# Performance work log

Hardware: AMD Instinct MI355X
Metric: run time of the kernel (lower is better)

Reference implementation:

```python
import jax, jax.numpy as jnp
import numpy as np

IN_DIM, H, E_DIM = 32, 64, 16
N_NODES, N_EDGES = 50000, 100000


def setup_inputs() -> dict:
    key = jax.random.key(0)
    ks = jax.random.split(key, 12)
    x = jax.random.normal(ks[0], (N_NODES, IN_DIM), dtype=jnp.float32)
    edge_index = jax.random.randint(ks[1], (2, N_EDGES), 0, N_NODES, dtype=jnp.int64)
    edge_attr = jax.random.uniform(ks[2], (N_EDGES, E_DIM), dtype=jnp.float32)
    def lin(k, fan_in, shape):
        return jax.random.normal(k, shape, dtype=jnp.float32) / np.sqrt(fan_in)
    return {
        "x": x,
        "edge_index": edge_index,
        "edge_attr": edge_attr,
        # lin0: Linear(in_dim, h)
        "lin0_w": lin(ks[3], IN_DIM, (H, IN_DIM)),
        "lin0_b": jnp.zeros((H,), jnp.float32),
        # NNConv's edge network: Linear(edge_dim, h*h)
        "nn_w": lin(ks[4], E_DIM, (H * H, E_DIM)),
        "nn_b": jnp.zeros((H * H,), jnp.float32),
        # NNConv root weight [in_ch, out_ch] and bias
        "root": lin(ks[5], H, (H, H)),
        "conv_b": jnp.zeros((H,), jnp.float32),
        # GRU (single layer): weight_ih [3h,h], weight_hh [3h,h], biases [3h]
        "w_ih": lin(ks[6], H, (3 * H, H)),
        "w_hh": lin(ks[7], H, (3 * H, H)),
        "b_ih": jnp.zeros((3 * H,), jnp.float32),
        "b_hh": jnp.zeros((3 * H,), jnp.float32),
    }


def _nnconv(x, src, dst, edge_attr, nn_w, nn_b, root, conv_b, num_nodes):
    # per-edge weight matrices [E, h_in, h_out] from the edge MLP
    W_e = (edge_attr @ nn_w.T + nn_b).reshape(-1, H, H)
    # gather source features, per-edge matvec, scatter-add to destinations
    msg = jnp.einsum('ei,eio->eo', x[src], W_e)          # [E, h]
    agg = jax.ops.segment_sum(msg, dst, num_segments=num_nodes)
    return agg + x @ root + conv_b


def _gru_step(x, h, w_ih, w_hh, b_ih, b_hh):
    gi = x @ w_ih.T + b_ih                                # [N, 3h]
    gh = h @ w_hh.T + b_hh
    i_r, i_z, i_n = jnp.split(gi, 3, axis=-1)
    h_r, h_z, h_n = jnp.split(gh, 3, axis=-1)
    r = jax.nn.sigmoid(i_r + h_r)
    z = jax.nn.sigmoid(i_z + h_z)
    n = jnp.tanh(i_n + r * h_n)
    return (1.0 - z) * n + z * h


def reference(x, edge_index, edge_attr, lin0_w, lin0_b, nn_w, nn_b,
              root, conv_b, w_ih, w_hh, b_ih, b_hh):
    src, dst = edge_index[0], edge_index[1]
    num_nodes = x.shape[0]
    out = jax.nn.relu(x @ lin0_w.T + lin0_b)              # [N, h]
    h = out
    for _ in range(3):
        m = jax.nn.relu(_nnconv(out, src, dst, edge_attr, nn_w, nn_b,
                                root, conv_b, num_nodes))
        h = _gru_step(m, h, w_ih, w_hh, b_ih, b_hh)
        out = h
    return out
```

## Files before the change

kernel.cpp:

```cpp
#include <hip/hip_runtime.h>
#include <hip/hip_bf16.h>

typedef unsigned short u16;
typedef __attribute__((ext_vector_type(8))) _Float16 h8v;
typedef __attribute__((ext_vector_type(4))) float f32x4;

#define CAP 32

static __device__ __forceinline__ u16 f2h(float f) {
    _Float16 h = (_Float16)f;
    u16 r; __builtin_memcpy(&r, &h, 2); return r;
}
static __device__ __forceinline__ float h2f(u16 b) {
    _Float16 h; __builtin_memcpy(&h, &b, 2); return (float)h;
}
static __device__ __forceinline__ float sigm(float x) {
    return 1.f / (1.f + __expf(-x));
}
static __device__ __forceinline__ float tanh_f(float x) {
    return 1.f - 2.f / (__expf(2.f * x) + 1.f);
}

__global__ __launch_bounds__(256) void k_prep(
        const float* __restrict__ nn_w, const float* __restrict__ nn_b,
        const float* __restrict__ root, const float* __restrict__ w_hh,
        const float* __restrict__ w_ih, const float* __restrict__ lin0_w,
        const float* __restrict__ ea,
        u16* __restrict__ wf2, u16* __restrict__ w1, u16* __restrict__ w2,
        u16* __restrict__ w0, u16* __restrict__ ea16, int* __restrict__ deg,
        int N, int nEA) {
    int idx = blockIdx.x * 256 + threadIdx.x;
    if (idx < 34 * 4 * 512) {
        int j = idx & 7, lane = (idx >> 3) & 63;
        int rest = idx >> 9;
        int ct = rest & 3, kc = rest >> 2;
        int kappa = kc * 32 + ((lane >> 4) * 8) + j;
        int o = ct * 16 + (lane & 15);
        float v;
        if (kappa < 1024) {
            int k = kappa >> 6, i = kappa & 63;
            v = nn_w[(size_t)(i * 64 + o) * 16 + k];
        } else {
            v = nn_b[(size_t)(kappa - 1024) * 64 + o];
        }
        wf2[idx] = f2h(v);
    }
    if (idx < 16384 + 12288 + 2048) {
        if (idx < 16384) {
            int j = idx & 7, lane = (idx >> 3) & 63;
            int rest = idx >> 9;
            int ct = rest & 15, kc = rest >> 4;
            int k = kc * 32 + ((lane >> 4) * 8) + j;
            int col = ct * 16 + (lane & 15);
            float v = (col < 64) ? root[(size_t)k * 64 + col]
                                 : w_hh[(size_t)(col - 64) * 64 + k];
            w1[idx] = f2h(v);
        } else if (idx < 16384 + 12288) {
            int i2 = idx - 16384;
            int j = i2 & 7, lane = (i2 >> 3) & 63;
            int rest = i2 >> 9;
            int ct = rest % 12, kc = rest / 12;
            int k = kc * 32 + ((lane >> 4) * 8) + j;
            int col = ct * 16 + (lane & 15);
            w2[i2] = f2h(w_ih[(size_t)col * 64 + k]);
        } else {
            int i3 = idx - 16384 - 12288;
            int j = i3 & 7, lane = (i3 >> 3) & 63;
            int ct = i3 >> 9;
            int k = ((lane >> 4) * 8) + j;
            int col = ct * 16 + (lane & 15);
            w0[i3] = f2h(lin0_w[(size_t)col * 32 + k]);
        }
    }
    if (idx < N) deg[idx] = 0;
    if (idx < nEA) ea16[idx] = f2h(ea[idx]);
}

__global__ __launch_bounds__(256) void k_build(
        const int* __restrict__ ei, int* __restrict__ deg,
        int* __restrict__ tab, int E) {
    int e = blockIdx.x * 256 + threadIdx.x;
    if (e < E) {
        int dst = ei[E + e];
        int pos = atomicAdd(&deg[dst], 1);
        if (pos < CAP) tab[(size_t)dst * CAP + pos] = e;
    }
}

__global__ __launch_bounds__(256) void k_lin0(
        const float* __restrict__ x, const u16* __restrict__ w0,
        const float* __restrict__ b, float* __restrict__ out, int N) {
    int t = threadIdx.x, l = t & 63, w = t >> 6, g = l >> 4;
    int n0 = blockIdx.x * 64 + w * 16;
    int node = n0 + (l & 15);
    int nc = node < N ? node : N - 1;
    const float* xrow = x + (size_t)nc * 32 + g * 8;
    float4 xa = *(const float4*)(xrow);
    float4 xb = *(const float4*)(xrow + 4);
    h8v xh;
    xh[0] = (_Float16)xa.x; xh[1] = (_Float16)xa.y;
    xh[2] = (_Float16)xa.z; xh[3] = (_Float16)xa.w;
    xh[4] = (_Float16)xb.x; xh[5] = (_Float16)xb.y;
    xh[6] = (_Float16)xb.z; xh[7] = (_Float16)xb.w;

    f32x4 acc[4];
    #pragma unroll
    for (int ct = 0; ct < 4; ct++) {
        h8v wh = *(const h8v*)((const _Float16*)w0 + (ct * 64 + l) * 8);
        acc[ct] = __builtin_amdgcn_mfma_f32_16x16x32_f16(wh, xh, (f32x4)(0.f), 0, 0, 0);
    }
    if (node < N) {
        #pragma unroll
        for (int ct = 0; ct < 4; ct++) {
            int c = ct * 16 + g * 4;
            f32x4 bb = *(const f32x4*)(b + c);
            f32x4 ov;
            #pragma unroll
            for (int r = 0; r < 4; r++) ov[r] = fmaxf(acc[ct][r] + bb[r], 0.f);
            *(f32x4*)(out + (size_t)node * 64 + c) = ov;
        }
    }
}

__global__ __launch_bounds__(256) void k_AB(
        const float* __restrict__ x, const u16* __restrict__ ea16,
        const u16* __restrict__ wf2, const int* __restrict__ ei,
        u16* __restrict__ msg, int E) {
    int t = threadIdx.x, l = t & 63, w = t >> 6, g = l >> 4;
    int eblk = blockIdx.x * 256 + w * 64;

    int eact[4];
    h8v xf0[4], xf1[4], eav[4][2];
    #pragma unroll
    for (int et = 0; et < 4; et++) {
        int e = eblk + et * 16 + (l & 15);
        eact[et] = e;
        int ec = e < E ? e : E - 1;
        int src = ei[ec];
        const float* xr = x + (size_t)src * 64 + g * 8;
        float4 v0 = *(const float4*)(xr);
        float4 v1 = *(const float4*)(xr + 4);
        float4 v2 = *(const float4*)(xr + 32);
        float4 v3 = *(const float4*)(xr + 36);
        h8v a, b;
        a[0] = (_Float16)v0.x; a[1] = (_Float16)v0.y;
        a[2] = (_Float16)v0.z; a[3] = (_Float16)v0.w;
        a[4] = (_Float16)v1.x; a[5] = (_Float16)v1.y;
        a[6] = (_Float16)v1.z; a[7] = (_Float16)v1.w;
        b[0] = (_Float16)v2.x; b[1] = (_Float16)v2.y;
        b[2] = (_Float16)v2.z; b[3] = (_Float16)v2.w;
        b[4] = (_Float16)v3.x; b[5] = (_Float16)v3.y;
        b[6] = (_Float16)v3.z; b[7] = (_Float16)v3.w;
        xf0[et] = a;
        xf1[et] = b;
        const _Float16* ep = (const _Float16*)ea16 + (size_t)ec * 16;
        eav[et][0] = *(const h8v*)(ep);
        eav[et][1] = *(const h8v*)(ep + 8);
    }

    f32x4 acc[4][4];
    #pragma unroll
    for (int et = 0; et < 4; et++)
        #pragma unroll
        for (int ct = 0; ct < 4; ct++) acc[et][ct] = (f32x4)(0.f);

    const _Float16* wfh = (const _Float16*)wf2;

    #pragma unroll
    for (int p = 0; p < 8; p++) {
        #pragma unroll
        for (int kcl = 0; kcl < 4; kcl++) {
            int kc = p * 4 + kcl;
            h8v af[4];
            #pragma unroll
            for (int ct = 0; ct < 4; ct++)
                af[ct] = *(const h8v*)(wfh + (size_t)(kc * 4 + ct) * 512 + l * 8);
            #pragma unroll
            for (int et = 0; et < 4; et++) {
                _Float16 s = (kcl < 2) ? eav[et][p >> 2][(2 * p) & 7]
                                       : eav[et][p >> 2][(2 * p + 1) & 7];
                h8v es = {s, s, s, s, s, s, s, s};
                h8v zf = es * ((kcl & 1) ? xf1[et] : xf0[et]);
                #pragma unroll
                for (int ct = 0; ct < 4; ct++)
                    acc[et][ct] = __builtin_amdgcn_mfma_f32_16x16x32_f16(af[ct], zf, acc[et][ct], 0, 0, 0);
            }
        }
    }
    #pragma unroll
    for (int kcl = 0; kcl < 2; kcl++) {
        int kc = 32 + kcl;
        h8v af[4];
        #pragma unroll
        for (int ct = 0; ct < 4; ct++)
            af[ct] = *(const h8v*)(wfh + (size_t)(kc * 4 + ct) * 512 + l * 8);
        #pragma unroll
        for (int et = 0; et < 4; et++) {
            h8v zf = (kcl & 1) ? xf1[et] : xf0[et];
            #pragma unroll
            for (int ct = 0; ct < 4; ct++)
                acc[et][ct] = __builtin_amdgcn_mfma_f32_16x16x32_f16(af[ct], zf, acc[et][ct], 0, 0, 0);
        }
    }

    #pragma unroll
    for (int et = 0; et < 4; et++) {
        int e = eact[et];
        if (e < E) {
            u16* mr = msg + (size_t)e * 64 + g * 4;
            #pragma unroll
            for (int ct = 0; ct < 4; ct++) {
                ushort4 pk;
                pk.x = f2h(acc[et][ct][0]);
                pk.y = f2h(acc[et][ct][1]);
                pk.z = f2h(acc[et][ct][2]);
                pk.w = f2h(acc[et][ct][3]);
                *(ushort4*)(mr + ct * 16) = pk;
            }
        }
    }
}

__global__ __launch_bounds__(256) void k_C(
        const float* __restrict__ x, const u16* __restrict__ msg,
        const int* __restrict__ deg, const int* __restrict__ tab,
        const u16* __restrict__ w1, const u16* __restrict__ w2,
        const float* __restrict__ conv_b, const float* __restrict__ b_hh,
        const float* __restrict__ b_ih, float* __restrict__ hout, int N) {
    __shared__ float mld[4][16][68];
    int t = threadIdx.x, l = t & 63, w = t >> 6, g = l >> 4;
    int n0 = blockIdx.x * 64 + w * 16;
    int node = n0 + (l & 15);
    int nc = node < N ? node : N - 1;
    const float* xrow = x + (size_t)nc * 64 + g * 8;
    const _Float16* w1h = (const _Float16*)w1;
    const _Float16* w2h = (const _Float16*)w2;

    h8v xh[2];
    #pragma unroll
    for (int kc = 0; kc < 2; kc++) {
        f32x4 a = *(const f32x4*)(xrow + kc * 32);
        f32x4 b = *(const f32x4*)(xrow + kc * 32 + 4);
        #pragma unroll
        for (int j = 0; j < 8; j++) xh[kc][j] = (_Float16)(j < 4 ? a[j] : b[j - 4]);
    }

    f32x4 avs[4];
    #pragma unroll
    for (int ct = 0; ct < 4; ct++) avs[ct] = (f32x4)(0.f);
    if (node < N) {
        int dg = deg[node];
        dg = dg < CAP ? dg : CAP;
        const int* tr = tab + (size_t)node * CAP;
        for (int j = 0; j < dg; j++) {
            int eid = tr[j];
            const u16* mr = msg + (size_t)eid * 64 + g * 4;
            #pragma unroll
            for (int ct = 0; ct < 4; ct++) {
                ushort4 mv = *(const ushort4*)(mr + ct * 16);
                avs[ct][0] += h2f(mv.x);
                avs[ct][1] += h2f(mv.y);
                avs[ct][2] += h2f(mv.z);
                avs[ct][3] += h2f(mv.w);
            }
        }
    }

    f32x4 acc1[16];
    #pragma unroll
    for (int ct = 0; ct < 16; ct++) acc1[ct] = (f32x4)(0.f);
    #pragma unroll
    for (int kc = 0; kc < 2; kc++) {
        #pragma unroll
        for (int ct = 0; ct < 16; ct++) {
            h8v wh = *(const h8v*)(w1h + (size_t)(kc * 16 + ct) * 512 + l * 8);
            acc1[ct] = __builtin_amdgcn_mfma_f32_16x16x32_f16(wh, xh[kc], acc1[ct], 0, 0, 0);
        }
    }

    #pragma unroll
    for (int ct = 0; ct < 4; ct++) {
        int c = ct * 16 + g * 4;
        f32x4 cb = *(const f32x4*)(conv_b + c);
        f32x4 mv;
        #pragma unroll
        for (int r = 0; r < 4; r++) mv[r] = fmaxf(acc1[ct][r] + avs[ct][r] + cb[r], 0.f);
        *(f32x4*)(&mld[w][l & 15][c]) = mv;
    }
    #pragma unroll
    for (int ct = 4; ct < 16; ct++) {
        int c = (ct - 4) * 16 + g * 4;
        f32x4 bh = *(const f32x4*)(b_hh + c);
        #pragma unroll
        for (int r = 0; r < 4; r++) acc1[ct][r] += bh[r];
    }
    __syncthreads();

    h8v mh[2];
    #pragma unroll
    for (int kc = 0; kc < 2; kc++) {
        const float* mr = &mld[w][l & 15][kc * 32 + g * 8];
        f32x4 a = *(const f32x4*)(mr);
        f32x4 b = *(const f32x4*)(mr + 4);
        #pragma unroll
        for (int j = 0; j < 8; j++) mh[kc][j] = (_Float16)(j < 4 ? a[j] : b[j - 4]);
    }

    f32x4 acc2[12];
    #pragma unroll
    for (int ct = 0; ct < 12; ct++) acc2[ct] = (f32x4)(0.f);
    #pragma unroll
    for (int kc = 0; kc < 2; kc++) {
        #pragma unroll
        for (int ct = 0; ct < 12; ct++) {
            h8v wh = *(const h8v*)(w2h + (size_t)(kc * 12 + ct) * 512 + l * 8);
            acc2[ct] = __builtin_amdgcn_mfma_f32_16x16x32_f16(wh, mh[kc], acc2[ct], 0, 0, 0);
        }
    }

    #pragma unroll
    for (int q = 0; q < 4; q++) {
        int c = q * 16 + g * 4;
        f32x4 bir = *(const f32x4*)(b_ih + c);
        f32x4 biz = *(const f32x4*)(b_ih + 64 + c);
        f32x4 bin = *(const f32x4*)(b_ih + 128 + c);
        f32x4 hv = (f32x4)(0.f);
        if (node < N) hv = *(const f32x4*)(x + (size_t)node * 64 + c);
        f32x4 outv;
        #pragma unroll
        for (int r = 0; r < 4; r++) {
            float rr = sigm(acc2[q][r] + bir[r] + acc1[4 + q][r]);
            float zz = sigm(acc2[4 + q][r] + biz[r] + acc1[8 + q][r]);
            float nt = tanh_f(acc2[8 + q][r] + bin[r] + rr * acc1[12 + q][r]);
            outv[r] = (1.f - zz) * nt + zz * hv[r];
        }
        if (node < N) *(f32x4*)(hout + (size_t)node * 64 + c) = outv;
    }
}

extern "C" void kernel_launch(void* const* d_in, const int* in_sizes, int n_in,
                              void* d_out, int out_size, void* d_ws, size_t ws_size,
                              hipStream_t stream) {
    const float* x_in   = (const float*)d_in[0];
    const int*   ei     = (const int*)d_in[1];
    const float* ea     = (const float*)d_in[2];
    const float* lin0_w = (const float*)d_in[3];
    const float* lin0_b = (const float*)d_in[4];
    const float* nn_w   = (const float*)d_in[5];
    const float* nn_b   = (const float*)d_in[6];
    const float* root   = (const float*)d_in[7];
    const float* conv_b = (const float*)d_in[8];
    const float* w_ih   = (const float*)d_in[9];
    const float* w_hh   = (const float*)d_in[10];
    const float* b_ih   = (const float*)d_in[11];
    const float* b_hh   = (const float*)d_in[12];

    int N = in_sizes[0] / 32;
    int E = in_sizes[1] / 2;

    char* ws = (char*)d_ws;
    size_t off = 0;
    auto alloc = [&](size_t bytes) { char* p = ws + off; off += (bytes + 255) & ~(size_t)255; return p; };
    float* xbuf   = (float*)alloc((size_t)N * 64 * 4);
    u16*   msg    = (u16*)alloc((size_t)E * 64 * 2);
    u16*   wf2    = (u16*)alloc((size_t)34 * 4 * 512 * 2);
    u16*   ea16   = (u16*)alloc((size_t)E * 16 * 2);
    u16*   w1     = (u16*)alloc(16384 * 2);
    u16*   w2     = (u16*)alloc(12288 * 2);
    u16*   w0     = (u16*)alloc(2048 * 2);
    int*   deg    = (int*)alloc((size_t)N * 4);
    int*   tab    = (int*)alloc((size_t)N * CAP * 4);
    (void)ws_size;

    int nEA = E * 16;
    hipLaunchKernelGGL(k_prep, dim3((nEA + 255) / 256), dim3(256), 0, stream,
                       nn_w, nn_b, root, w_hh, w_ih, lin0_w, ea,
                       wf2, w1, w2, w0, ea16, deg, N, nEA);
    hipLaunchKernelGGL(k_build, dim3((E + 255) / 256), dim3(256), 0, stream, ei, deg, tab, E);
    hipLaunchKernelGGL(k_lin0, dim3((N + 63) / 64), dim3(256), 0, stream, x_in, w0, lin0_b, xbuf, N);

    for (int it = 0; it < 3; it++) {
        hipLaunchKernelGGL(k_AB, dim3((E + 255) / 256), dim3(256), 0, stream,
                           xbuf, ea16, wf2, ei, msg, E);
        float* hout = (it == 2) ? (float*)d_out : xbuf;
        hipLaunchKernelGGL(k_C, dim3((N + 63) / 64), dim3(256), 0, stream, xbuf, msg,
                           deg, tab, w1, w2, conv_b, b_hh, b_ih, hout, N);
    }
}
```

Measured before the change: 178.0 us.

## Stage edge-network weights through LDS with register prefetch in k_AB

The edge-message kernel now copies the fused edge-network weight tiles from global memory into a 16KB shared-memory buffer in chunks. The next chunk is prefetched into registers while MFMAs consume the current one, and each wave reads its A fragments from LDS instead of global/L2. Each wave now handles 32 edges instead of 64, halving accumulators and doubling the grid. The goal is to reduce redundant global weight loads and register pressure, at the cost of two block barriers per chunk and less weight reuse per wave.

```diff
diff --git a/kernel.cpp b/kernel.cpp
--- a/kernel.cpp
+++ b/kernel.cpp
@@ -126,13 +126,14 @@
         const float* __restrict__ x, const u16* __restrict__ ea16,
         const u16* __restrict__ wf2, const int* __restrict__ ei,
         u16* __restrict__ msg, int E) {
+    __shared__ __align__(16) u16 Ab[8192];
     int t = threadIdx.x, l = t & 63, w = t >> 6, g = l >> 4;
-    int eblk = blockIdx.x * 256 + w * 64;
-
-    int eact[4];
-    h8v xf0[4], xf1[4], eav[4][2];
-    #pragma unroll
-    for (int et = 0; et < 4; et++) {
+    int eblk = blockIdx.x * 128 + w * 32;
+
+    int eact[2];
+    h8v xf0[2], xf1[2], eav[2][2];
+    #pragma unroll
+    for (int et = 0; et < 2; et++) {
         int e = eblk + et * 16 + (l & 15);
         eact[et] = e;
         int ec = e < E ? e : E - 1;
@@ -158,27 +159,45 @@
         eav[et][1] = *(const h8v*)(ep + 8);
     }
 
-    f32x4 acc[4][4];
-    #pragma unroll
-    for (int et = 0; et < 4; et++)
+    f32x4 acc[2][4];
+    #pragma unroll
+    for (int et = 0; et < 2; et++)
         #pragma unroll
         for (int ct = 0; ct < 4; ct++) acc[et][ct] = (f32x4)(0.f);
 
-    const _Float16* wfh = (const _Float16*)wf2;
+    const uint4* wf2u = (const uint4*)wf2;
+    uint4* Abu = (uint4*)Ab;
+    const _Float16* AbH = (const _Float16*)Ab;
+
+    {
+        uint4 s0[4];
+        #pragma unroll
+        for (int i = 0; i < 4; i++) s0[i] = wf2u[t + i * 256];
+        #pragma unroll
+        for (int i = 0; i < 4; i++) Abu[t + i * 256] = s0[i];
+    }
+    __syncthreads();
 
     #pragma unroll
     for (int p = 0; p < 8; p++) {
+        uint4 st[4];
+        if (p < 7) {
+            #pragma unroll
+            for (int i = 0; i < 4; i++) st[i] = wf2u[(p + 1) * 1024 + t + i * 256];
+        } else {
+            st[0] = wf2u[8 * 1024 + t];
+            st[1] = wf2u[8 * 1024 + 256 + t];
+        }
         #pragma unroll
         for (int kcl = 0; kcl < 4; kcl++) {
-            int kc = p * 4 + kcl;
             h8v af[4];
             #pragma unroll
             for (int ct = 0; ct < 4; ct++)
-                af[ct] = *(const h8v*)(wfh + (size_t)(kc * 4 + ct) * 512 + l * 8);
-            #pragma unroll
-            for (int et = 0; et < 4; et++) {
-                _Float16 s = (kcl < 2) ? eav[et][p >> 2][(2 * p) & 7]
-                                       : eav[et][p >> 2][(2 * p + 1) & 7];
+                af[ct] = *(const h8v*)(AbH + (kcl * 4 + ct) * 512 + l * 8);
+            const int k = 2 * p + (kcl >> 1);
+            #pragma unroll
+            for (int et = 0; et < 2; et++) {
+                _Float16 s = eav[et][k >> 3][k & 7];
                 h8v es = {s, s, s, s, s, s, s, s};
                 h8v zf = es * ((kcl & 1) ? xf1[et] : xf0[et]);
                 #pragma unroll
@@ -186,16 +205,25 @@
                     acc[et][ct] = __builtin_amdgcn_mfma_f32_16x16x32_f16(af[ct], zf, acc[et][ct], 0, 0, 0);
             }
         }
-    }
+        __syncthreads();
+        if (p < 7) {
+            #pragma unroll
+            for (int i = 0; i < 4; i++) Abu[t + i * 256] = st[i];
+        } else {
+            Abu[t] = st[0];
+            Abu[256 + t] = st[1];
+        }
+        __syncthreads();
+    }
+
     #pragma unroll
     for (int kcl = 0; kcl < 2; kcl++) {
-        int kc = 32 + kcl;
         h8v af[4];
         #pragma unroll
         for (int ct = 0; ct < 4; ct++)
-            af[ct] = *(const h8v*)(wfh + (size_t)(kc * 4 + ct) * 512 + l * 8);
-        #pragma unroll
-        for (int et = 0; et < 4; et++) {
+            af[ct] = *(const h8v*)(AbH + (kcl * 4 + ct) * 512 + l * 8);
+        #pragma unroll
+        for (int et = 0; et < 2; et++) {
             h8v zf = (kcl & 1) ? xf1[et] : xf0[et];
             #pragma unroll
             for (int ct = 0; ct < 4; ct++)
@@ -204,7 +232,7 @@
     }
 
     #pragma unroll
-    for (int et = 0; et < 4; et++) {
+    for (int et = 0; et < 2; et++) {
         int e = eact[et];
         if (e < E) {
             u16* mr = msg + (size_t)e * 64 + g * 4;
@@ -380,7 +408,7 @@
     hipLaunchKernelGGL(k_lin0, dim3((N + 63) / 64), dim3(256), 0, stream, x_in, w0, lin0_b, xbuf, N);
 
     for (int it = 0; it < 3; it++) {
-        hipLaunchKernelGGL(k_AB, dim3((E + 255) / 256), dim3(256), 0, stream,
+        hipLaunchKernelGGL(k_AB, dim3((E + 127) / 128), dim3(256), 0, stream,
                            xbuf, ea16, wf2, ei, msg, E);
         float* hout = (it == 2) ? (float*)d_out : xbuf;
         hipLaunchKernelGGL(k_C, dim3((N + 63) / 64), dim3(256), 0, stream, xbuf, msg,
```

New measurement: 240.5 us. 1.35x slower.

## Fuse per-edge message compute into node aggregation+GRU kernel via shared-memory tiles

Applied to the files above, without the earlier changes.

Fuses the edge-message kernel and the node aggregation/GRU kernel into one per-node-tile kernel. Each block prefix-sums the degrees of its 64 nodes and computes the messages for their incoming edges with MFMA into an LDS tile, then reduces them without going through a global msg buffer. It also merges the edge-table build and lin0 kernels into one launch, and ping-pongs node buffers so reads and writes do not alias. This removes the global message round-trip and some launches. In exchange it adds block syncs, a serial edge-list fill done by one wavefront, per-block load imbalance, and fewer blocks (N/64) doing the edge MFMA work.

```diff
diff --git a/kernel.cpp b/kernel.cpp
--- a/kernel.cpp
+++ b/kernel.cpp
@@ -6,6 +6,7 @@
 typedef __attribute__((ext_vector_type(4))) float f32x4;
 
 #define CAP 32
+#define ECAP 256
 
 static __device__ __forceinline__ u16 f2h(float f) {
     _Float16 h = (_Float16)f;
@@ -76,25 +77,29 @@
     if (idx < nEA) ea16[idx] = f2h(ea[idx]);
 }
 
-__global__ __launch_bounds__(256) void k_build(
-        const int* __restrict__ ei, int* __restrict__ deg,
-        int* __restrict__ tab, int E) {
-    int e = blockIdx.x * 256 + threadIdx.x;
-    if (e < E) {
-        int dst = ei[E + e];
-        int pos = atomicAdd(&deg[dst], 1);
-        if (pos < CAP) tab[(size_t)dst * CAP + pos] = e;
-    }
-}
-
-__global__ __launch_bounds__(256) void k_lin0(
-        const float* __restrict__ x, const u16* __restrict__ w0,
-        const float* __restrict__ b, float* __restrict__ out, int N) {
-    int t = threadIdx.x, l = t & 63, w = t >> 6, g = l >> 4;
-    int n0 = blockIdx.x * 64 + w * 16;
+__global__ __launch_bounds__(256) void k_pre2(
+        const int* __restrict__ ei, int* __restrict__ deg, int* __restrict__ tab,
+        const float* __restrict__ x_in, const u16* __restrict__ w0,
+        const float* __restrict__ lin0_b, float* __restrict__ x0,
+        int N, int E) {
+    int nbuild = (E + 255) / 256;
+    int bid = blockIdx.x;
+    int t = threadIdx.x;
+    if (bid < nbuild) {
+        int e = bid * 256 + t;
+        if (e < E) {
+            int dst = ei[E + e];
+            int pos = atomicAdd(&deg[dst], 1);
+            if (pos < CAP) tab[(size_t)dst * CAP + pos] = e;
+        }
+        return;
+    }
+    int b2 = bid - nbuild;
+    int l = t & 63, w = t >> 6, g = l >> 4;
+    int n0 = b2 * 64 + w * 16;
     int node = n0 + (l & 15);
     int nc = node < N ? node : N - 1;
-    const float* xrow = x + (size_t)nc * 32 + g * 8;
+    const float* xrow = x_in + (size_t)nc * 32 + g * 8;
     float4 xa = *(const float4*)(xrow);
     float4 xb = *(const float4*)(xrow + 4);
     h8v xh;
@@ -102,7 +107,6 @@
     xh[2] = (_Float16)xa.z; xh[3] = (_Float16)xa.w;
     xh[4] = (_Float16)xb.x; xh[5] = (_Float16)xb.y;
     xh[6] = (_Float16)xb.z; xh[7] = (_Float16)xb.w;
-
     f32x4 acc[4];
     #pragma unroll
     for (int ct = 0; ct < 4; ct++) {
@@ -113,129 +117,49 @@
         #pragma unroll
         for (int ct = 0; ct < 4; ct++) {
             int c = ct * 16 + g * 4;
-            f32x4 bb = *(const f32x4*)(b + c);
+            f32x4 bb = *(const f32x4*)(lin0_b + c);
             f32x4 ov;
             #pragma unroll
             for (int r = 0; r < 4; r++) ov[r] = fmaxf(acc[ct][r] + bb[r], 0.f);
-            *(f32x4*)(out + (size_t)node * 64 + c) = ov;
-        }
-    }
-}
-
-__global__ __launch_bounds__(256) void k_AB(
-        const float* __restrict__ x, const u16* __restrict__ ea16,
-        const u16* __restrict__ wf2, const int* __restrict__ ei,
-        u16* __restrict__ msg, int E) {
+            *(f32x4*)(x0 + (size_t)node * 64 + c) = ov;
+        }
+    }
+}
+
+__global__ __launch_bounds__(256) void k_ABC(
+        const float* __restrict__ xA, float* __restrict__ hout,
+        const int* __restrict__ ei, const u16* __restrict__ ea16,
+        const u16* __restrict__ wf2, const u16* __restrict__ w1,
+        const u16* __restrict__ w2, const int* __restrict__ deg,
+        const int* __restrict__ tab, const float* __restrict__ conv_b,
+        const float* __restrict__ b_hh, const float* __restrict__ b_ih,
+        int N, int E) {
+    __shared__ __align__(16) u16 mtile[ECAP * 68];
+    __shared__ int els[ECAP];
+    __shared__ int offs[65];
     int t = threadIdx.x, l = t & 63, w = t >> 6, g = l >> 4;
-    int eblk = blockIdx.x * 256 + w * 64;
-
-    int eact[4];
-    h8v xf0[4], xf1[4], eav[4][2];
-    #pragma unroll
-    for (int et = 0; et < 4; et++) {
-        int e = eblk + et * 16 + (l & 15);
-        eact[et] = e;
-        int ec = e < E ? e : E - 1;
-        int src = ei[ec];
-        const float* xr = x + (size_t)src * 64 + g * 8;
-        float4 v0 = *(const float4*)(xr);
-        float4 v1 = *(const float4*)(xr + 4);
-        float4 v2 = *(const float4*)(xr + 32);
-        float4 v3 = *(const float4*)(xr + 36);
-        h8v a, b;
-        a[0] = (_Float16)v0.x; a[1] = (_Float16)v0.y;
-        a[2] = (_Float16)v0.z; a[3] = (_Float16)v0.w;
-        a[4] = (_Float16)v1.x; a[5] = (_Float16)v1.y;
-        a[6] = (_Float16)v1.z; a[7] = (_Float16)v1.w;
-        b[0] = (_Float16)v2.x; b[1] = (_Float16)v2.y;
-        b[2] = (_Float16)v2.z; b[3] = (_Float16)v2.w;
-        b[4] = (_Float16)v3.x; b[5] = (_Float16)v3.y;
-        b[6] = (_Float16)v3.z; b[7] = (_Float16)v3.w;
-        xf0[et] = a;
-        xf1[et] = b;
-        const _Float16* ep = (const _Float16*)ea16 + (size_t)ec * 16;
-        eav[et][0] = *(const h8v*)(ep);
-        eav[et][1] = *(const h8v*)(ep + 8);
-    }
-
-    f32x4 acc[4][4];
-    #pragma unroll
-    for (int et = 0; et < 4; et++)
-        #pragma unroll
-        for (int ct = 0; ct < 4; ct++) acc[et][ct] = (f32x4)(0.f);
-
-    const _Float16* wfh = (const _Float16*)wf2;
-
-    #pragma unroll
-    for (int p = 0; p < 8; p++) {
-        #pragma unroll
-        for (int kcl = 0; kcl < 4; kcl++) {
-            int kc = p * 4 + kcl;
-            h8v af[4];
-            #pragma unroll
-            for (int ct = 0; ct < 4; ct++)
-                af[ct] = *(const h8v*)(wfh + (size_t)(kc * 4 + ct) * 512 + l * 8);
-            #pragma unroll
-            for (int et = 0; et < 4; et++) {
-                _Float16 s = (kcl < 2) ? eav[et][p >> 2][(2 * p) & 7]
-                                       : eav[et][p >> 2][(2 * p + 1) & 7];
-                h8v es = {s, s, s, s, s, s, s, s};
-                h8v zf = es * ((kcl & 1) ? xf1[et] : xf0[et]);
-                #pragma unroll
-                for (int ct = 0; ct < 4; ct++)
-                    acc[et][ct] = __builtin_amdgcn_mfma_f32_16x16x32_f16(af[ct], zf, acc[et][ct], 0, 0, 0);
-            }
-        }
-    }
-    #pragma unroll
-    for (int kcl = 0; kcl < 2; kcl++) {
-        int kc = 32 + kcl;
-        h8v af[4];
-        #pragma unroll
-        for (int ct = 0; ct < 4; ct++)
-            af[ct] = *(const h8v*)(wfh + (size_t)(kc * 4 + ct) * 512 + l * 8);
-        #pragma unroll
-        for (int et = 0; et < 4; et++) {
-            h8v zf = (kcl & 1) ? xf1[et] : xf0[et];
-            #pragma unroll
-            for (int ct = 0; ct < 4; ct++)
-                acc[et][ct] = __builtin_amdgcn_mfma_f32_16x16x32_f16(af[ct], zf, acc[et][ct], 0, 0, 0);
-        }
-    }
-
-    #pragma unroll
-    for (int et = 0; et < 4; et++) {
-        int e = eact[et];
-        if (e < E) {
-            u16* mr = msg + (size_t)e * 64 + g * 4;
-            #pragma unroll
-            for (int ct = 0; ct < 4; ct++) {
-                ushort4 pk;
-                pk.x = f2h(acc[et][ct][0]);
-                pk.y = f2h(acc[et][ct][1]);
-                pk.z = f2h(acc[et][ct][2]);
-                pk.w = f2h(acc[et][ct][3]);
-                *(ushort4*)(mr + ct * 16) = pk;
-            }
-        }
-    }
-}
-
-__global__ __launch_bounds__(256) void k_C(
-        const float* __restrict__ x, const u16* __restrict__ msg,
-        const int* __restrict__ deg, const int* __restrict__ tab,
-        const u16* __restrict__ w1, const u16* __restrict__ w2,
-        const float* __restrict__ conv_b, const float* __restrict__ b_hh,
-        const float* __restrict__ b_ih, float* __restrict__ hout, int N) {
-    __shared__ float mld[4][16][68];
-    int t = threadIdx.x, l = t & 63, w = t >> 6, g = l >> 4;
-    int n0 = blockIdx.x * 64 + w * 16;
-    int node = n0 + (l & 15);
+    int n0 = blockIdx.x * 64;
+    int nb = w * 16 + (l & 15);
+    int node = n0 + nb;
     int nc = node < N ? node : N - 1;
-    const float* xrow = x + (size_t)nc * 64 + g * 8;
-    const _Float16* w1h = (const _Float16*)w1;
-    const _Float16* w2h = (const _Float16*)w2;
-
+
+    if (w == 0) {
+        int nd = n0 + l;
+        int d = 0;
+        if (nd < N) { d = deg[nd]; if (d > CAP) d = CAP; }
+        int s = d;
+        #pragma unroll
+        for (int o = 1; o < 64; o <<= 1) {
+            int v = __shfl_up(s, o, 64);
+            if (l >= o) s += v;
+        }
+        offs[l + 1] = s;
+        if (l == 0) offs[0] = 0;
+    }
+    __syncthreads();
+    int T_e = offs[64];
+
+    const float* xrow = xA + (size_t)nc * 64 + g * 8;
     h8v xh[2];
     #pragma unroll
     for (int kc = 0; kc < 2; kc++) {
@@ -248,23 +172,148 @@
     f32x4 avs[4];
     #pragma unroll
     for (int ct = 0; ct < 4; ct++) avs[ct] = (f32x4)(0.f);
-    if (node < N) {
-        int dg = deg[node];
-        dg = dg < CAP ? dg : CAP;
-        const int* tr = tab + (size_t)node * CAP;
-        for (int j = 0; j < dg; j++) {
-            int eid = tr[j];
-            const u16* mr = msg + (size_t)eid * 64 + g * 4;
+
+    const _Float16* wfh = (const _Float16*)wf2;
+
+    for (int base = 0; base < T_e; base += ECAP) {
+        int cnt = T_e - base; if (cnt > ECAP) cnt = ECAP;
+        if (w == 0) {
+            int nd = n0 + l;
+            int d = 0;
+            if (nd < N) { d = deg[nd]; if (d > CAP) d = CAP; }
+            int o = offs[l];
+            const int* tr = tab + (size_t)(nd < N ? nd : 0) * CAP;
+            for (int j = 0; j < d; j++) {
+                int s = o + j - base;
+                if (s >= 0 && s < ECAP) els[s] = tr[j];
+            }
+        }
+        __syncthreads();
+
+        int ntiles = (cnt + 15) >> 4;
+        bool val[4];
+        int slots[4];
+        h8v xf0[4], xf1[4], eav[4][2];
+        #pragma unroll
+        for (int et = 0; et < 4; et++) {
+            int tile = w + et * 4;
+            val[et] = (tile < ntiles);
+            int slot = tile * 16 + (l & 15);
+            slots[et] = slot;
+            int sv = slot < cnt ? slot : cnt - 1;
+            if (val[et]) {
+                int e = els[sv];
+                int src = ei[e];
+                const float* xr = xA + (size_t)src * 64 + g * 8;
+                float4 v0 = *(const float4*)(xr);
+                float4 v1 = *(const float4*)(xr + 4);
+                float4 v2 = *(const float4*)(xr + 32);
+                float4 v3 = *(const float4*)(xr + 36);
+                h8v a, b;
+                a[0] = (_Float16)v0.x; a[1] = (_Float16)v0.y;
+                a[2] = (_Float16)v0.z; a[3] = (_Float16)v0.w;
+                a[4] = (_Float16)v1.x; a[5] = (_Float16)v1.y;
+                a[6] = (_Float16)v1.z; a[7] = (_Float16)v1.w;
+                b[0] = (_Float16)v2.x; b[1] = (_Float16)v2.y;
+                b[2] = (_Float16)v2.z; b[3] = (_Float16)v2.w;
+                b[4] = (_Float16)v3.x; b[5] = (_Float16)v3.y;
+                b[6] = (_Float16)v3.z; b[7] = (_Float16)v3.w;
+                xf0[et] = a;
+                xf1[et] = b;
+                const _Float16* ep = (const _Float16*)ea16 + (size_t)e * 16;
+                eav[et][0] = *(const h8v*)(ep);
+                eav[et][1] = *(const h8v*)(ep + 8);
+            }
+        }
+
+        f32x4 acc[4][4];
+        #pragma unroll
+        for (int et = 0; et < 4; et++)
             #pragma unroll
-            for (int ct = 0; ct < 4; ct++) {
-                ushort4 mv = *(const ushort4*)(mr + ct * 16);
-                avs[ct][0] += h2f(mv.x);
-                avs[ct][1] += h2f(mv.y);
-                avs[ct][2] += h2f(mv.z);
-                avs[ct][3] += h2f(mv.w);
-            }
-        }
-    }
+            for (int ct = 0; ct < 4; ct++) acc[et][ct] = (f32x4)(0.f);
+
+        if (val[0]) {
+            #pragma unroll
+            for (int p = 0; p < 8; p++) {
+                #pragma unroll
+                for (int kcl = 0; kcl < 4; kcl++) {
+                    int kc = p * 4 + kcl;
+                    h8v af[4];
+                    #pragma unroll
+                    for (int ct = 0; ct < 4; ct++)
+                        af[ct] = *(const h8v*)(wfh + (size_t)(kc * 4 + ct) * 512 + l * 8);
+                    const int k = 2 * p + (kcl >> 1);
+                    #pragma unroll
+                    for (int et = 0; et < 4; et++) {
+                        if (val[et]) {
+                            _Float16 s = eav[et][k >> 3][k & 7];
+                            h8v es = {s, s, s, s, s, s, s, s};
+                            h8v zf = es * ((kcl & 1) ? xf1[et] : xf0[et]);
+                            #pragma unroll
+                            for (int ct = 0; ct < 4; ct++)
+                                acc[et][ct] = __builtin_amdgcn_mfma_f32_16x16x32_f16(af[ct], zf, acc[et][ct], 0, 0, 0);
+                        }
+                    }
+                }
+            }
+            #pragma unroll
+            for (int kcl = 0; kcl < 2; kcl++) {
+                int kc = 32 + kcl;
+                h8v af[4];
+                #pragma unroll
+                for (int ct = 0; ct < 4; ct++)
+                    af[ct] = *(const h8v*)(wfh + (size_t)(kc * 4 + ct) * 512 + l * 8);
+                #pragma unroll
+                for (int et = 0; et < 4; et++) {
+                    if (val[et]) {
+                        h8v zf = (kcl & 1) ? xf1[et] : xf0[et];
+                        #pragma unroll
+                        for (int ct = 0; ct < 4; ct++)
+                            acc[et][ct] = __builtin_amdgcn_mfma_f32_16x16x32_f16(af[ct], zf, acc[et][ct], 0, 0, 0);
+                    }
+                }
+            }
+            #pragma unroll
+            for (int et = 0; et < 4; et++) {
+                if (val[et]) {
+                    u16* mr = &mtile[(size_t)slots[et] * 68 + g * 4];
+                    #pragma unroll
+                    for (int ct = 0; ct < 4; ct++) {
+                        ushort4 pk;
+                        pk.x = f2h(acc[et][ct][0]);
+                        pk.y = f2h(acc[et][ct][1]);
+                        pk.z = f2h(acc[et][ct][2]);
+                        pk.w = f2h(acc[et][ct][3]);
+                        *(ushort4*)(mr + ct * 16) = pk;
+                    }
+                }
+            }
+        }
+        __syncthreads();
+
+        {
+            int o = offs[nb], d2 = offs[nb + 1] - o;
+            for (int j = 0; j < d2; j++) {
+                int s = o + j - base;
+                if (s >= 0 && s < cnt) {
+                    const u16* mr = &mtile[(size_t)s * 68 + g * 4];
+                    #pragma unroll
+                    for (int ct = 0; ct < 4; ct++) {
+                        ushort4 mv = *(const ushort4*)(mr + ct * 16);
+                        avs[ct][0] += h2f(mv.x);
+                        avs[ct][1] += h2f(mv.y);
+                        avs[ct][2] += h2f(mv.z);
+                        avs[ct][3] += h2f(mv.w);
+                    }
+                }
+            }
+        }
+        __syncthreads();
+    }
+
+    const _Float16* w1h = (const _Float16*)w1;
+    const _Float16* w2h = (const _Float16*)w2;
+    float* mld = (float*)mtile;
 
     f32x4 acc1[16];
     #pragma unroll
@@ -285,7 +334,7 @@
         f32x4 mv;
         #pragma unroll
         for (int r = 0; r < 4; r++) mv[r] = fmaxf(acc1[ct][r] + avs[ct][r] + cb[r], 0.f);
-        *(f32x4*)(&mld[w][l & 15][c]) = mv;
+        *(f32x4*)(&mld[(size_t)nb * 68 + c]) = mv;
     }
     #pragma unroll
     for (int ct = 4; ct < 16; ct++) {
@@ -299,7 +348,7 @@
     h8v mh[2];
     #pragma unroll
     for (int kc = 0; kc < 2; kc++) {
-        const float* mr = &mld[w][l & 15][kc * 32 + g * 8];
+        const float* mr = &mld[(size_t)nb * 68 + kc * 32 + g * 8];
         f32x4 a = *(const f32x4*)(mr);
         f32x4 b = *(const f32x4*)(mr + 4);
         #pragma unroll
@@ -325,7 +374,7 @@
         f32x4 biz = *(const f32x4*)(b_ih + 64 + c);
         f32x4 bin = *(const f32x4*)(b_ih + 128 + c);
         f32x4 hv = (f32x4)(0.f);
-        if (node < N) hv = *(const f32x4*)(x + (size_t)node * 64 + c);
+        if (node < N) hv = *(const f32x4*)(xA + (size_t)node * 64 + c);
         f32x4 outv;
         #pragma unroll
         for (int r = 0; r < 4; r++) {
@@ -361,8 +410,8 @@
     char* ws = (char*)d_ws;
     size_t off = 0;
     auto alloc = [&](size_t bytes) { char* p = ws + off; off += (bytes + 255) & ~(size_t)255; return p; };
-    float* xbuf   = (float*)alloc((size_t)N * 64 * 4);
-    u16*   msg    = (u16*)alloc((size_t)E * 64 * 2);
+    float* x0     = (float*)alloc((size_t)N * 64 * 4);
+    float* x1     = (float*)alloc((size_t)N * 64 * 4);
     u16*   wf2    = (u16*)alloc((size_t)34 * 4 * 512 * 2);
     u16*   ea16   = (u16*)alloc((size_t)E * 16 * 2);
     u16*   w1     = (u16*)alloc(16384 * 2);
@@ -373,17 +422,21 @@
     (void)ws_size;
 
     int nEA = E * 16;
+    int nbuild = (E + 255) / 256;
+    int ntile  = (N + 63) / 64;
+
     hipLaunchKernelGGL(k_prep, dim3((nEA + 255) / 256), dim3(256), 0, stream,
                        nn_w, nn_b, root, w_hh, w_ih, lin0_w, ea,
                        wf2, w1, w2, w0, ea16, deg, N, nEA);
-    hipLaunchKernelGGL(k_build, dim3((E + 255) / 256), dim3(256), 0, stream, ei, deg, tab, E);
-    hipLaunchKernelGGL(k_lin0, dim3((N + 63) / 64), dim3(256), 0, stream, x_in, w0, lin0_b, xbuf, N);
-
+    hipLaunchKernelGGL(k_pre2, dim3(nbuild + ntile), dim3(256), 0, stream,
+                       ei, deg, tab, x_in, w0, lin0_b, x0, N, E);
+
+    float* bufs[4] = {x0, x1, x0, (float*)d_out};
     for (int it = 0; it < 3; it++) {
-        hipLaunchKernelGGL(k_AB, dim3((E + 255) / 256), dim3(256), 0, stream,
-                           xbuf, ea16, wf2, ei, msg, E);
-        float* hout = (it == 2) ? (float*)d_out : xbuf;
-        hipLaunchKernelGGL(k_C, dim3((N + 63) / 64), dim3(256), 0, stream, xbuf, msg,
-                           deg, tab, w1, w2, conv_b, b_hh, b_ih, hout, N);
-    }
-}
+        float* xA   = bufs[it & 1];
+        float* hout = (it == 2) ? (float*)d_out : bufs[(it + 1) & 1];
+        hipLaunchKernelGGL(k_ABC, dim3(ntile), dim3(256), 0, stream,
+                           xA, hout, ei, ea16, wf2, w1, w2, deg, tab,
+                           conv_b, b_hh, b_ih, N, E);
+    }
+}
```

New measurement: 289.2 us. +62.5%, slower.
